# Optimization experiments

Measured on AMD Instinct MI355X. Metric: run time of the kernel, lower is better.

The kernel has to match this reference:

```python
import jax, jax.numpy as jnp
import numpy as np

B, T, NS, NC, M = 256, 128, 12, 4, 6
MU = 0.1                 # barrier parameter alg.mu
REG_BASE = 1.6           # fp.reg_exp_base
REG = 2.0                # bp.reg
REG_FAC = REG_BASE ** REG - 1.0


def _mt(a):
    return jnp.swapaxes(a, -1, -2)


def setup_inputs():
    key = jax.random.key(0)
    k = jax.random.split(key, 18)
    rn = lambda i, shape: jax.random.normal(k[i], shape, dtype=jnp.float32)
    eye_s = jnp.eye(NS, dtype=jnp.float32)
    eye_c = jnp.eye(NC, dtype=jnp.float32)
    fx = 0.9 * eye_s + 0.02 * rn(0, (B, T, NS, NS))
    fu = 0.1 * rn(1, (B, T, NS, NC))
    fxx = 0.01 * rn(2, (B, T, NS, NS, NS))
    fxu = 0.01 * rn(3, (B, T, NS, NS, NC))
    fuu = 0.01 * rn(4, (B, T, NS, NC, NC))
    qx = 0.1 * rn(5, (B, T, NS))
    qu = 0.1 * rn(6, (B, T, NC))
    Ax = 0.1 * rn(7, (B, T, NS, NS))
    qxx = eye_s + Ax @ _mt(Ax)            # PSD stage cost Hessian
    Au = 0.1 * rn(8, (B, T, NC, NC))
    quu = eye_c + Au @ _mt(Au)            # PD control Hessian
    qxu = 0.05 * rn(9, (B, T, NS, NC))
    cx = 0.1 * rn(10, (B, T, M, NS))
    cu = 0.1 * rn(11, (B, T, M, NC))
    # feasible iterate: c < 0 strictly, dual s > 0
    c = -(jax.random.uniform(k[12], (B, T, M), dtype=jnp.float32) + 0.1)
    s = 0.05 + 0.1 * jax.random.uniform(k[13], (B, T, M), dtype=jnp.float32)
    px = 0.1 * rn(14, (B, NS))
    P = 0.1 * rn(15, (B, NS, NS))
    pxx = eye_s + P @ _mt(P)              # PSD terminal Hessian
    return {"qx": qx, "qu": qu, "qxx": qxx, "qxu": qxu, "quu": quu,
            "fx": fx, "fu": fu, "fxx": fxx, "fxu": fxu, "fuu": fuu,
            "cx": cx, "cu": cu, "c": c, "s": s, "px": px, "pxx": pxx}


def _backward_pass(qx, qu, qxx, qxu, quu, fx, fu, fxx, fxu, fuu, cx, cu, c, s, px, pxx):
    """Feasible-branch ipddp Riccati backward recursion over T steps, batched over B."""
    Bsz = qx.shape[0]

    def step(carry, inp):
        Vx, Vxx, dV0, dV1, qu_err, mu_err = carry
        (qx_t, qu_t, qxx_t, qxu_t, quu_t, fx_t, fu_t,
         fxx_t, fxu_t, fuu_t, cx_t, cu_t, c_t, s_t) = inp
        s_col = s_t[..., None]                      # (B,M,1)
        c_col = c_t[..., None]                      # (B,M,1)
        # Q-function expansions
        Qx = qx_t[..., None] + _mt(cx_t) @ s_col + _mt(fx_t) @ Vx       # (B,NS,1)
        Qu = qu_t[..., None] + _mt(cu_t) @ s_col + _mt(fu_t) @ Vx       # (B,NC,1)
        fxV = _mt(fx_t) @ Vxx
        v = Vx[..., 0]                              # (B,NS)
        Qxx = qxx_t + fxV @ fx_t + jnp.einsum('bs,bsij->bij', v, fxx_t)
        Qxu = qxu_t + fxV @ fu_t + jnp.einsum('bs,bsij->bij', v, fxu_t)
        Quu = quu_t + _mt(fu_t) @ Vxx @ fu_t + jnp.einsum('bs,bsij->bij', v, fuu_t)
        Quu = 0.5 * (Quu + _mt(Quu))
        Quu_reg = Quu + quu_t * REG_FAC
        # interior-point (feasible) modifications
        r = s_col * c_col + MU                      # (B,M,1)
        cinv = 1.0 / c_col
        sc = (s_t / c_t)[..., None]                 # diag(SCinv) entries
        SCcu = sc * cu_t                            # SCinv @ cu
        SCcx = sc * cx_t                            # SCinv @ cx
        cuSCcu = _mt(cu_t) @ SCcu
        Qu = Qu - _mt(cu_t) @ (cinv * r)
        tempQux = _mt(Qxu) - _mt(cu_t) @ SCcx       # (B,NC,NS)
        rhs = jnp.concatenate([Qu, tempQux], axis=-1)   # (B,NC,1+NS)
        kK = -jnp.linalg.solve(Quu_reg - cuSCcu, rhs)
        ku = kK[..., :1]                            # (B,NC,1)
        Ku = kK[..., 1:]                            # (B,NC,NS)
        cuku = cu_t @ ku                            # (B,M,1)
        ks = (-cinv * (r + s_col * cuku))[..., 0]   # (B,M)
        Ks = -(sc * (cx_t + cu_t @ Ku))             # (B,M,NS)
        Quu2 = Quu - cuSCcu
        Qxu2 = _mt(tempQux)
        Qxx2 = Qxx - _mt(cx_t) @ SCcx
        Qx2 = Qx - _mt(cx_t) @ (cinv * r)
        dV0 = dV0 + (_mt(ku) @ Qu)[..., 0, 0]
        dV1 = dV1 + 0.5 * (_mt(ku) @ Quu2 @ ku)[..., 0, 0]
        QxuKu = Qxu2 @ Ku
        KtQ = _mt(Ku) @ Quu2
        Vx_new = Qx2 + _mt(Ku) @ Qu + KtQ @ ku + Qxu2 @ ku
        Vxx_new = Qxx2 + _mt(QxuKu) + QxuKu + KtQ @ Ku
        Vxx_new = 0.5 * (Vxx_new + _mt(Vxx_new))
        qu_err = jnp.maximum(qu_err, jnp.max(jnp.abs(Qu)))
        mu_err = jnp.maximum(mu_err, jnp.max(jnp.abs(r)))
        return (Vx_new, Vxx_new, dV0, dV1, qu_err, mu_err), (ku[..., 0], Ku, ks, Ks)

    xs = tuple(jnp.moveaxis(a, 1, 0) for a in
               (qx, qu, qxx, qxu, quu, fx, fu, fxx, fxu, fuu, cx, cu, c, s))
    zero = jnp.zeros((), jnp.float32)
    init = (px[..., None], pxx, jnp.zeros((Bsz,), jnp.float32),
            jnp.zeros((Bsz,), jnp.float32), zero, zero)
    carry, outs = jax.lax.scan(step, init, xs, reverse=True)
    Vx, Vxx, dV0, dV1, qu_err, mu_err = carry
    ku, Ku, ks, Ks = (jnp.moveaxis(o, 0, 1) for o in outs)
    dV = jnp.stack([dV0, dV1], axis=-1)             # (B,2)
    opterr = jnp.maximum(qu_err, mu_err)            # c_err == 0 in feasible branch
    return ku, Ku, ks, Ks, dV, opterr, Vx[..., 0], Vxx


def reference(qx, qu, qxx, qxu, quu, fx, fu, fxx, fxu, fuu, cx, cu, c, s, px, pxx):
    return _backward_pass(qx, qu, qxx, qxu, quu, fx, fu, fxx, fxu, fuu,
                          cx, cu, c, s, px, pxx)
```

## Files before the change

kernel.cpp:

```cpp
#include <hip/hip_runtime.h>
#include <cstdint>
#include <cstddef>

#define B_  256
#define T_  128
#define NS_ 12
#define NC_ 4
#define M_  6

constexpr float MU_F      = 0.1f;
constexpr float REG_FAC_F = (float)(1.6 * 1.6 - 1.0);

#define OF_FX   0
#define OF_FU   144
#define OF_FXX  192
#define OF_FXU  1920
#define OF_FUU  2496
#define OF_QXX  2688
#define OF_QXU  2832
#define OF_QUU  2880
#define OF_QX   2896
#define OF_QU   2908
#define OF_CX   2912
#define OF_CU   2984
#define OF_C    3008
#define OF_S    3014
#define STG_N   3020

#define O_KU    0
#define O_KUBIG 131072
#define O_KS    1703936
#define O_KSBIG 1900544
#define O_DV    4259840
#define O_OPT   4260352
#define O_VX    4260353
#define O_VXX   4263425

__device__ __forceinline__ void bar_lds() {
    asm volatile("s_waitcnt lgkmcnt(0)\n\ts_barrier" ::: "memory");
}

__device__ __forceinline__ void gl_lds16(const float* g, float* l) {
    __builtin_amdgcn_global_load_lds((const __attribute__((address_space(1))) void*)g,
                                     (__attribute__((address_space(3))) void*)l, 16, 0, 0);
}
__device__ __forceinline__ void gl_lds4(const float* g, float* l) {
    __builtin_amdgcn_global_load_lds((const __attribute__((address_space(1))) void*)g,
                                     (__attribute__((address_space(3))) void*)l, 4, 0, 0);
}

__global__ __launch_bounds__(256) void ddp_backward(
    const float* __restrict__ qx,  const float* __restrict__ qu,
    const float* __restrict__ qxx, const float* __restrict__ qxu,
    const float* __restrict__ quu, const float* __restrict__ fx,
    const float* __restrict__ fu,  const float* __restrict__ fxx,
    const float* __restrict__ fxu, const float* __restrict__ fuu,
    const float* __restrict__ cx,  const float* __restrict__ cu,
    const float* __restrict__ c_,  const float* __restrict__ s_,
    const float* __restrict__ px,  const float* __restrict__ pxx,
    float* __restrict__ out, float* __restrict__ ws)
{
    const int tid  = threadIdx.x;
    const int b    = blockIdx.x;
    const int lane = tid & 63;
    const int wv   = tid >> 6;

    __shared__ float stg[2][STG_N];
    __shared__ float sVx[12], sVxx[144];
    __shared__ float sfxV[144], sfuV[48];
    __shared__ float sQxx[144], sQxu[48];
    __shared__ float sQuuR[16], sQuu2[16], sM4[16];
    __shared__ float stQux[48];
    __shared__ float sQxb[12], sQub[4], sQu[4], sQx2[12];
    __shared__ float sr[6], scinv[6], ssc[6];
    __shared__ float sKu[48], sku[4], sKtQ[48];
    __shared__ float sAcc[4];

    const float* srcs[14] = {qx, qu, qxx, qxu, quu, fx, fu, fxx, fxu, fuu, cx, cu, c_, s_};

    auto prefetch = [&](float* dst, int tt) {
        const size_t bt = (size_t)b * T_ + tt;
        constexpr int ch_arr[22]  = {5,6,7,7,7,7,7,7,7,8,8,8,9,2,3,4,0,1,10,11,12,13};
        constexpr int ch_goff[22] = {0,0,0,256,512,768,1024,1280,1536,0,256,512,0,0,0,0,0,0,0,0,0,0};
        constexpr int ch_loff[22] = {OF_FX, OF_FU,
                                     OF_FXX, OF_FXX+256, OF_FXX+512, OF_FXX+768,
                                     OF_FXX+1024, OF_FXX+1280, OF_FXX+1536,
                                     OF_FXU, OF_FXU+256, OF_FXU+512,
                                     OF_FUU, OF_QXX, OF_QXU, OF_QUU, OF_QX, OF_QU,
                                     OF_CX, OF_CU, OF_C, OF_S};
        constexpr int ch_nb[22]   = {576,192,1024,1024,1024,1024,1024,1024,768,
                                     1024,1024,256,768,576,192,64,48,16,288,96,24,24};
        constexpr int sl[14]      = {12,4,144,48,16,144,48,1728,576,192,72,24,6,6};
        #pragma unroll
        for (int ci = 0; ci < 22; ++ci) {
            if ((ci & 3) == wv) {
                const float* g = srcs[ch_arr[ci]] + bt * (size_t)sl[ch_arr[ci]] + ch_goff[ci];
                float* l = dst + ch_loff[ci];
                if ((ch_nb[ci] & 15) == 0) {
                    if (lane * 16 < ch_nb[ci]) gl_lds16(g + lane * 4, l);
                } else {
                    if (lane * 4  < ch_nb[ci]) gl_lds4 (g + lane,     l);
                }
            }
        }
    };

    if (tid < 144) sVxx[tid] = pxx[(size_t)b * 144 + tid];
    if (tid < 12)  sVx[tid]  = px[(size_t)b * 12 + tid];
    if (tid == 0)  { sAcc[0] = 0.f; sAcc[1] = 0.f; sAcc[2] = 0.f; sAcc[3] = 0.f; }
    prefetch(stg[0], T_ - 1);
    __syncthreads();

    int cur = 0;
    for (int t = T_ - 1; t >= 0; --t) {
        const float* S = stg[cur];
        if (t > 0) prefetch(stg[cur ^ 1], t - 1);
        const size_t bt = (size_t)b * T_ + t;

        if (tid < 144) {
            const int i = tid / 12, k = tid % 12;
            float acc = 0.f;
            #pragma unroll
            for (int m = 0; m < 12; ++m) acc += S[OF_FX + m*12 + i] * sVxx[m*12 + k];
            sfxV[tid] = acc;
        } else if (tid < 192) {
            const int idx = tid - 144, a = idx / 12, k = idx % 12;
            float acc = 0.f;
            #pragma unroll
            for (int m = 0; m < 12; ++m) acc += S[OF_FU + m*4 + a] * sVxx[m*12 + k];
            sfuV[idx] = acc;
        } else if (tid < 198) {
            const int k = tid - 192;
            const float cc = S[OF_C + k], ssv = S[OF_S + k];
            sr[k] = ssv * cc + MU_F;
            scinv[k] = 1.0f / cc;
            ssc[k] = ssv / cc;
        } else if (tid < 210) {
            const int i = tid - 198;
            float acc = S[OF_QX + i];
            #pragma unroll
            for (int k = 0; k < 6; ++k)  acc += S[OF_CX + k*12 + i] * S[OF_S + k];
            #pragma unroll
            for (int m = 0; m < 12; ++m) acc += S[OF_FX + m*12 + i] * sVx[m];
            sQxb[i] = acc;
        } else if (tid < 214) {
            const int a = tid - 210;
            float acc = S[OF_QU + a];
            #pragma unroll
            for (int k = 0; k < 6; ++k)  acc += S[OF_CU + k*4 + a] * S[OF_S + k];
            #pragma unroll
            for (int m = 0; m < 12; ++m) acc += S[OF_FU + m*4 + a] * sVx[m];
            sQub[a] = acc;
        }
        bar_lds();

        if (tid < 144) {
            const int i = tid / 12, j = tid % 12; (void)j;
            float acc = S[OF_QXX + tid];
            #pragma unroll
            for (int k = 0; k < 12; ++k) acc += sfxV[i*12 + k] * S[OF_FX + k*12 + (tid % 12)];
            #pragma unroll
            for (int ss2 = 0; ss2 < 12; ++ss2) acc += sVx[ss2] * S[OF_FXX + ss2*144 + tid];
            sQxx[tid] = acc;
        } else if (tid < 192) {
            const int idx = tid - 144, i = idx / 4, j = idx % 4;
            float acc = S[OF_QXU + idx];
            #pragma unroll
            for (int k = 0; k < 12; ++k) acc += sfxV[i*12 + k] * S[OF_FU + k*4 + j];
            #pragma unroll
            for (int ss2 = 0; ss2 < 12; ++ss2) acc += sVx[ss2] * S[OF_FXU + ss2*48 + idx];
            sQxu[idx] = acc;
        } else if (tid < 208) {
            const int idx = tid - 192, a = idx / 4, b2 = idx % 4;
            float acc = S[OF_QUU + idx];
            #pragma unroll
            for (int k = 0; k < 12; ++k) acc += sfuV[a*12 + k] * S[OF_FU + k*4 + b2];
            #pragma unroll
            for (int ss2 = 0; ss2 < 12; ++ss2) acc += sVx[ss2] * S[OF_FUU + ss2*16 + idx];
            sQuuR[idx] = acc;
        }
        bar_lds();

        if (tid < 144) {
            const int i = tid / 12, j = tid % 12;
            float acc = sQxx[tid];
            #pragma unroll
            for (int k = 0; k < 6; ++k) acc -= S[OF_CX + k*12 + i] * ssc[k] * S[OF_CX + k*12 + j];
            sQxx[tid] = acc;
        } else if (tid < 192) {
            const int idx = tid - 144, a = idx / 12, i = idx % 12;
            float acc = sQxu[i*4 + a];
            #pragma unroll
            for (int k = 0; k < 6; ++k) acc -= S[OF_CU + k*4 + a] * ssc[k] * S[OF_CX + k*12 + i];
            stQux[idx] = acc;
        } else if (tid < 208) {
            const int idx = tid - 192, a = idx / 4, b2 = idx % 4;
            const float q = 0.5f * (sQuuR[idx] + sQuuR[b2*4 + a]);
            float cs = 0.f;
            #pragma unroll
            for (int k = 0; k < 6; ++k) cs += ssc[k] * S[OF_CU + k*4 + a] * S[OF_CU + k*4 + b2];
            const float q2 = q - cs;
            sQuu2[idx] = q2;
            sM4[idx]   = q2 + S[OF_QUU + idx] * REG_FAC_F;
        } else if (tid < 212) {
            const int a = tid - 208;
            float acc = sQub[a];
            #pragma unroll
            for (int k = 0; k < 6; ++k) acc -= S[OF_CU + k*4 + a] * scinv[k] * sr[k];
            sQu[a] = acc;
        } else if (tid < 224) {
            const int i = tid - 212;
            float acc = sQxb[i];
            #pragma unroll
            for (int k = 0; k < 6; ++k) acc -= S[OF_CX + k*12 + i] * scinv[k] * sr[k];
            sQx2[i] = acc;
        }
        bar_lds();

        if (tid < 13) {
            float a00=sM4[0],  a01=sM4[1],  a02=sM4[2],  a03=sM4[3];
            float a10=sM4[4],  a11=sM4[5],  a12=sM4[6],  a13=sM4[7];
            float a20=sM4[8],  a21=sM4[9],  a22=sM4[10], a23=sM4[11];
            float a30=sM4[12], a31=sM4[13], a32=sM4[14], a33=sM4[15];
            const float i0 = 1.0f / a00;
            const float l10 = a10*i0, l20 = a20*i0, l30 = a30*i0;
            a11 -= l10*a01; a12 -= l10*a02; a13 -= l10*a03;
            a21 -= l20*a01; a22 -= l20*a02; a23 -= l20*a03;
            a31 -= l30*a01; a32 -= l30*a02; a33 -= l30*a03;
            const float i1 = 1.0f / a11;
            const float l21 = a21*i1, l31 = a31*i1;
            a22 -= l21*a12; a23 -= l21*a13;
            a32 -= l31*a12; a33 -= l31*a13;
            const float i2 = 1.0f / a22;
            const float l32 = a32*i2;
            a33 -= l32*a23;

            float r0, r1, r2, r3;
            if (tid == 0) { r0 = sQu[0]; r1 = sQu[1]; r2 = sQu[2]; r3 = sQu[3]; }
            else { const int i = tid - 1; r0 = stQux[i]; r1 = stQux[12+i]; r2 = stQux[24+i]; r3 = stQux[36+i]; }

            const float y0 = r0;
            const float y1 = r1 - l10*y0;
            const float y2 = r2 - l20*y0 - l21*y1;
            const float y3 = r3 - l30*y0 - l31*y1 - l32*y2;
            float x3 = y3 / a33;
            float x2 = (y2 - a23*x3) * i2;
            float x1 = (y1 - a12*x2 - a13*x3) * i1;
            float x0 = (y0 - a01*x1 - a02*x2 - a03*x3) * i0;
            x0 = -x0; x1 = -x1; x2 = -x2; x3 = -x3;

            if (tid == 0) {
                sku[0]=x0; sku[1]=x1; sku[2]=x2; sku[3]=x3;
                float* kg = out + O_KU + bt*4;
                kg[0]=x0; kg[1]=x1; kg[2]=x2; kg[3]=x3;
            } else {
                const int i = tid - 1;
                sKu[i]=x0; sKu[12+i]=x1; sKu[24+i]=x2; sKu[36+i]=x3;
                float* Kg = out + O_KUBIG + bt*48;
                Kg[i]=x0; Kg[12+i]=x1; Kg[24+i]=x2; Kg[36+i]=x3;
            }
        }
        bar_lds();

        if (tid < 48) {
            const int i = tid / 4, a = tid % 4;
            float acc = 0.f;
            #pragma unroll
            for (int b2 = 0; b2 < 4; ++b2) acc += sKu[b2*12 + i] * sQuu2[b2*4 + a];
            sKtQ[tid] = acc;
        } else if (tid < 54) {
            const int k = tid - 48;
            float cuku = 0.f;
            #pragma unroll
            for (int a = 0; a < 4; ++a) cuku += S[OF_CU + k*4 + a] * sku[a];
            out[O_KS + bt*6 + k] = -scinv[k] * (sr[k] + S[OF_S + k] * cuku);
        } else if (tid < 126) {
            const int idx = tid - 54, k = idx / 12, i = idx % 12;
            float acc = S[OF_CX + k*12 + i];
            #pragma unroll
            for (int a = 0; a < 4; ++a) acc += S[OF_CU + k*4 + a] * sKu[a*12 + i];
            out[O_KSBIG + bt*72 + idx] = -(ssc[k] * acc);
        } else if (tid == 126) {
            float d = 0.f;
            #pragma unroll
            for (int a = 0; a < 4; ++a) d += sku[a] * sQu[a];
            sAcc[0] += d;
        } else if (tid == 127) {
            float d = 0.f;
            #pragma unroll
            for (int a = 0; a < 4; ++a)
                #pragma unroll
                for (int b2 = 0; b2 < 4; ++b2) d += sku[a] * sQuu2[a*4 + b2] * sku[b2];
            sAcc[1] += 0.5f * d;
        } else if (tid == 128) {
            float m = 0.f;
            #pragma unroll
            for (int a = 0; a < 4; ++a) m = fmaxf(m, fabsf(sQu[a]));
            sAcc[2] = fmaxf(sAcc[2], m);
        } else if (tid == 129) {
            float m = 0.f;
            #pragma unroll
            for (int k = 0; k < 6; ++k) m = fmaxf(m, fabsf(sr[k]));
            sAcc[3] = fmaxf(sAcc[3], m);
        }
        bar_lds();

        if (tid < 144) {
            const int i = tid / 12, j = tid % 12;
            const float v1 = sQxx[i*12 + j], v2 = sQxx[j*12 + i];
            float qk = 0.f, kk1 = 0.f, kk2 = 0.f;
            #pragma unroll
            for (int a = 0; a < 4; ++a) {
                const float kui = sKu[a*12 + i], kuj = sKu[a*12 + j];
                qk  += stQux[a*12 + i] * kuj + stQux[a*12 + j] * kui;
                kk1 += sKtQ[i*4 + a] * kuj;
                kk2 += sKtQ[j*4 + a] * kui;
            }
            sVxx[tid] = 0.5f * (v1 + v2) + qk + 0.5f * (kk1 + kk2);
        } else if (tid < 156) {
            const int i = tid - 144;
            float acc = sQx2[i];
            #pragma unroll
            for (int a = 0; a < 4; ++a)
                acc += sKu[a*12 + i] * sQu[a] + sKtQ[i*4 + a] * sku[a] + stQux[a*12 + i] * sku[a];
            sVx[i] = acc;
        }
        __syncthreads();
        cur ^= 1;
    }

    if (tid == 0) {
        out[O_DV + b*2 + 0] = sAcc[0];
        out[O_DV + b*2 + 1] = sAcc[1];
        ws[b] = fmaxf(sAcc[2], sAcc[3]);
    }
    if (tid < 12)  out[O_VX + b*12 + tid] = sVx[tid];
    if (tid < 144) out[O_VXX + (size_t)b*144 + tid] = sVxx[tid];
}

__global__ __launch_bounds__(256) void opt_reduce(const float* __restrict__ ws,
                                                  float* __restrict__ out)
{
    float v = ws[threadIdx.x];
    #pragma unroll
    for (int o = 32; o > 0; o >>= 1) v = fmaxf(v, __shfl_down(v, o, 64));
    __shared__ float m[4];
    if ((threadIdx.x & 63) == 0) m[threadIdx.x >> 6] = v;
    __syncthreads();
    if (threadIdx.x == 0) out[O_OPT] = fmaxf(fmaxf(m[0], m[1]), fmaxf(m[2], m[3]));
}

extern "C" void kernel_launch(void* const* d_in, const int* in_sizes, int n_in,
                              void* d_out, int out_size, void* d_ws, size_t ws_size,
                              hipStream_t stream) {
    const float* qx  = (const float*)d_in[0];
    const float* qu  = (const float*)d_in[1];
    const float* qxx = (const float*)d_in[2];
    const float* qxu = (const float*)d_in[3];
    const float* quu = (const float*)d_in[4];
    const float* fx  = (const float*)d_in[5];
    const float* fu  = (const float*)d_in[6];
    const float* fxx = (const float*)d_in[7];
    const float* fxu = (const float*)d_in[8];
    const float* fuu = (const float*)d_in[9];
    const float* cx  = (const float*)d_in[10];
    const float* cu  = (const float*)d_in[11];
    const float* c_  = (const float*)d_in[12];
    const float* s_  = (const float*)d_in[13];
    const float* px  = (const float*)d_in[14];
    const float* pxx = (const float*)d_in[15];
    float* out = (float*)d_out;
    float* ws  = (float*)d_ws;

    hipLaunchKernelGGL(ddp_backward, dim3(B_), dim3(256), 0, stream,
                       qx, qu, qxx, qxu, quu, fx, fu, fxx, fxu, fuu,
                       cx, cu, c_, s_, px, pxx, out, ws);
    hipLaunchKernelGGL(opt_reduce, dim3(1), dim3(256), 0, stream, ws, out);
}
```

Measured before the change: 805.2 us.

## Collapse per-batch Riccati block to a single wavefront with fused phases

```diff
diff --git a/kernel.cpp b/kernel.cpp
--- a/kernel.cpp
+++ b/kernel.cpp
@@ -4,9 +4,6 @@
 
 #define B_  256
 #define T_  128
-#define NS_ 12
-#define NC_ 4
-#define M_  6
 
 constexpr float MU_F      = 0.1f;
 constexpr float REG_FAC_F = (float)(1.6 * 1.6 - 1.0);
@@ -36,10 +33,6 @@
 #define O_VX    4260353
 #define O_VXX   4263425
 
-__device__ __forceinline__ void bar_lds() {
-    asm volatile("s_waitcnt lgkmcnt(0)\n\ts_barrier" ::: "memory");
-}
-
 __device__ __forceinline__ void gl_lds16(const float* g, float* l) {
     __builtin_amdgcn_global_load_lds((const __attribute__((address_space(1))) void*)g,
                                      (__attribute__((address_space(3))) void*)l, 16, 0, 0);
@@ -48,8 +41,11 @@
     __builtin_amdgcn_global_load_lds((const __attribute__((address_space(1))) void*)g,
                                      (__attribute__((address_space(3))) void*)l, 4, 0, 0);
 }
-
-__global__ __launch_bounds__(256) void ddp_backward(
+__device__ __forceinline__ void wait_vm0() {
+    asm volatile("s_waitcnt vmcnt(0)" ::: "memory");
+}
+
+__global__ __launch_bounds__(64) void ddp_backward(
     const float* __restrict__ qx,  const float* __restrict__ qu,
     const float* __restrict__ qxx, const float* __restrict__ qxu,
     const float* __restrict__ quu, const float* __restrict__ fx,
@@ -60,25 +56,23 @@
     const float* __restrict__ px,  const float* __restrict__ pxx,
     float* __restrict__ out, float* __restrict__ ws)
 {
-    const int tid  = threadIdx.x;
+    const int lane = threadIdx.x;
     const int b    = blockIdx.x;
-    const int lane = tid & 63;
-    const int wv   = tid >> 6;
 
     __shared__ float stg[2][STG_N];
     __shared__ float sVx[12], sVxx[144];
     __shared__ float sfxV[144], sfuV[48];
-    __shared__ float sQxx[144], sQxu[48];
-    __shared__ float sQuuR[16], sQuu2[16], sM4[16];
-    __shared__ float stQux[48];
+    __shared__ float sQxx2[144], stQux[48], sGuu[16];
     __shared__ float sQxb[12], sQub[4], sQu[4], sQx2[12];
-    __shared__ float sr[6], scinv[6], ssc[6];
-    __shared__ float sKu[48], sku[4], sKtQ[48];
-    __shared__ float sAcc[4];
+    __shared__ float sr[6], scinv[6], ssc[6], sscr[6];
+    __shared__ float sKu[48], sku[4];
+    __shared__ float sErr[2];
+
+    float accDV0 = 0.f, accDV1 = 0.f, accQE = 0.f, accME = 0.f;
 
     const float* srcs[14] = {qx, qu, qxx, qxu, quu, fx, fu, fxx, fxu, fuu, cx, cu, c_, s_};
 
-    auto prefetch = [&](float* dst, int tt) {
+    auto stage_all = [&](float* dst, int tt) {
         const size_t bt = (size_t)b * T_ + tt;
         constexpr int ch_arr[22]  = {5,6,7,7,7,7,7,7,7,8,8,8,9,2,3,4,0,1,10,11,12,13};
         constexpr int ch_goff[22] = {0,0,0,256,512,768,1024,1280,1536,0,256,512,0,0,0,0,0,0,0,0,0,0};
@@ -93,249 +87,252 @@
         constexpr int sl[14]      = {12,4,144,48,16,144,48,1728,576,192,72,24,6,6};
         #pragma unroll
         for (int ci = 0; ci < 22; ++ci) {
-            if ((ci & 3) == wv) {
-                const float* g = srcs[ch_arr[ci]] + bt * (size_t)sl[ch_arr[ci]] + ch_goff[ci];
-                float* l = dst + ch_loff[ci];
-                if ((ch_nb[ci] & 15) == 0) {
-                    if (lane * 16 < ch_nb[ci]) gl_lds16(g + lane * 4, l);
-                } else {
-                    if (lane * 4  < ch_nb[ci]) gl_lds4 (g + lane,     l);
-                }
+            const float* g = srcs[ch_arr[ci]] + bt * (size_t)sl[ch_arr[ci]] + ch_goff[ci];
+            float* l = dst + ch_loff[ci];
+            if ((ch_nb[ci] & 15) == 0) {
+                if (lane * 16 < ch_nb[ci]) gl_lds16(g + lane * 4, l);
+            } else {
+                if (lane * 4  < ch_nb[ci]) gl_lds4 (g + lane,     l);
             }
         }
     };
 
-    if (tid < 144) sVxx[tid] = pxx[(size_t)b * 144 + tid];
-    if (tid < 12)  sVx[tid]  = px[(size_t)b * 12 + tid];
-    if (tid == 0)  { sAcc[0] = 0.f; sAcc[1] = 0.f; sAcc[2] = 0.f; sAcc[3] = 0.f; }
-    prefetch(stg[0], T_ - 1);
+    for (int e = lane; e < 144; e += 64) sVxx[e] = pxx[(size_t)b * 144 + e];
+    if (lane < 12) sVx[lane] = px[(size_t)b * 12 + lane];
+    stage_all(stg[0], T_ - 1);
+    wait_vm0();
     __syncthreads();
 
     int cur = 0;
     for (int t = T_ - 1; t >= 0; --t) {
         const float* S = stg[cur];
-        if (t > 0) prefetch(stg[cur ^ 1], t - 1);
+        if (t > 0) stage_all(stg[cur ^ 1], t - 1);
         const size_t bt = (size_t)b * T_ + t;
 
-        if (tid < 144) {
-            const int i = tid / 12, k = tid % 12;
-            float acc = 0.f;
-            #pragma unroll
-            for (int m = 0; m < 12; ++m) acc += S[OF_FX + m*12 + i] * sVxx[m*12 + k];
-            sfxV[tid] = acc;
-        } else if (tid < 192) {
-            const int idx = tid - 144, a = idx / 12, k = idx % 12;
-            float acc = 0.f;
-            #pragma unroll
-            for (int m = 0; m < 12; ++m) acc += S[OF_FU + m*4 + a] * sVxx[m*12 + k];
-            sfuV[idx] = acc;
-        } else if (tid < 198) {
-            const int k = tid - 192;
-            const float cc = S[OF_C + k], ssv = S[OF_S + k];
-            sr[k] = ssv * cc + MU_F;
-            scinv[k] = 1.0f / cc;
-            ssc[k] = ssv / cc;
-        } else if (tid < 210) {
-            const int i = tid - 198;
-            float acc = S[OF_QX + i];
-            #pragma unroll
-            for (int k = 0; k < 6; ++k)  acc += S[OF_CX + k*12 + i] * S[OF_S + k];
-            #pragma unroll
-            for (int m = 0; m < 12; ++m) acc += S[OF_FX + m*12 + i] * sVx[m];
-            sQxb[i] = acc;
-        } else if (tid < 214) {
-            const int a = tid - 210;
-            float acc = S[OF_QU + a];
-            #pragma unroll
-            for (int k = 0; k < 6; ++k)  acc += S[OF_CU + k*4 + a] * S[OF_S + k];
-            #pragma unroll
-            for (int m = 0; m < 12; ++m) acc += S[OF_FU + m*4 + a] * sVx[m];
-            sQub[a] = acc;
-        }
-        bar_lds();
-
-        if (tid < 144) {
-            const int i = tid / 12, j = tid % 12; (void)j;
-            float acc = S[OF_QXX + tid];
-            #pragma unroll
-            for (int k = 0; k < 12; ++k) acc += sfxV[i*12 + k] * S[OF_FX + k*12 + (tid % 12)];
-            #pragma unroll
-            for (int ss2 = 0; ss2 < 12; ++ss2) acc += sVx[ss2] * S[OF_FXX + ss2*144 + tid];
-            sQxx[tid] = acc;
-        } else if (tid < 192) {
-            const int idx = tid - 144, i = idx / 4, j = idx % 4;
-            float acc = S[OF_QXU + idx];
-            #pragma unroll
-            for (int k = 0; k < 12; ++k) acc += sfxV[i*12 + k] * S[OF_FU + k*4 + j];
-            #pragma unroll
-            for (int ss2 = 0; ss2 < 12; ++ss2) acc += sVx[ss2] * S[OF_FXU + ss2*48 + idx];
-            sQxu[idx] = acc;
-        } else if (tid < 208) {
-            const int idx = tid - 192, a = idx / 4, b2 = idx % 4;
-            float acc = S[OF_QUU + idx];
-            #pragma unroll
-            for (int k = 0; k < 12; ++k) acc += sfuV[a*12 + k] * S[OF_FU + k*4 + b2];
-            #pragma unroll
-            for (int ss2 = 0; ss2 < 12; ++ss2) acc += sVx[ss2] * S[OF_FUU + ss2*16 + idx];
-            sQuuR[idx] = acc;
-        }
-        bar_lds();
-
-        if (tid < 144) {
-            const int i = tid / 12, j = tid % 12;
-            float acc = sQxx[tid];
-            #pragma unroll
-            for (int k = 0; k < 6; ++k) acc -= S[OF_CX + k*12 + i] * ssc[k] * S[OF_CX + k*12 + j];
-            sQxx[tid] = acc;
-        } else if (tid < 192) {
-            const int idx = tid - 144, a = idx / 12, i = idx % 12;
-            float acc = sQxu[i*4 + a];
-            #pragma unroll
-            for (int k = 0; k < 6; ++k) acc -= S[OF_CU + k*4 + a] * ssc[k] * S[OF_CX + k*12 + i];
-            stQux[idx] = acc;
-        } else if (tid < 208) {
-            const int idx = tid - 192, a = idx / 4, b2 = idx % 4;
-            const float q = 0.5f * (sQuuR[idx] + sQuuR[b2*4 + a]);
-            float cs = 0.f;
-            #pragma unroll
-            for (int k = 0; k < 6; ++k) cs += ssc[k] * S[OF_CU + k*4 + a] * S[OF_CU + k*4 + b2];
-            const float q2 = q - cs;
-            sQuu2[idx] = q2;
-            sM4[idx]   = q2 + S[OF_QUU + idx] * REG_FAC_F;
-        } else if (tid < 212) {
-            const int a = tid - 208;
-            float acc = sQub[a];
-            #pragma unroll
-            for (int k = 0; k < 6; ++k) acc -= S[OF_CU + k*4 + a] * scinv[k] * sr[k];
-            sQu[a] = acc;
-        } else if (tid < 224) {
-            const int i = tid - 212;
-            float acc = sQxb[i];
-            #pragma unroll
-            for (int k = 0; k < 6; ++k) acc -= S[OF_CX + k*12 + i] * scinv[k] * sr[k];
-            sQx2[i] = acc;
-        }
-        bar_lds();
-
-        if (tid < 13) {
-            float a00=sM4[0],  a01=sM4[1],  a02=sM4[2],  a03=sM4[3];
-            float a10=sM4[4],  a11=sM4[5],  a12=sM4[6],  a13=sM4[7];
-            float a20=sM4[8],  a21=sM4[9],  a22=sM4[10], a23=sM4[11];
-            float a30=sM4[12], a31=sM4[13], a32=sM4[14], a33=sM4[15];
-            const float i0 = 1.0f / a00;
-            const float l10 = a10*i0, l20 = a20*i0, l30 = a30*i0;
-            a11 -= l10*a01; a12 -= l10*a02; a13 -= l10*a03;
-            a21 -= l20*a01; a22 -= l20*a02; a23 -= l20*a03;
-            a31 -= l30*a01; a32 -= l30*a02; a33 -= l30*a03;
-            const float i1 = 1.0f / a11;
-            const float l21 = a21*i1, l31 = a31*i1;
-            a22 -= l21*a12; a23 -= l21*a13;
-            a32 -= l31*a12; a33 -= l31*a13;
-            const float i2 = 1.0f / a22;
-            const float l32 = a32*i2;
-            a33 -= l32*a23;
-
-            float r0, r1, r2, r3;
-            if (tid == 0) { r0 = sQu[0]; r1 = sQu[1]; r2 = sQu[2]; r3 = sQu[3]; }
-            else { const int i = tid - 1; r0 = stQux[i]; r1 = stQux[12+i]; r2 = stQux[24+i]; r3 = stQux[36+i]; }
-
-            const float y0 = r0;
-            const float y1 = r1 - l10*y0;
-            const float y2 = r2 - l20*y0 - l21*y1;
-            const float y3 = r3 - l30*y0 - l31*y1 - l32*y2;
-            float x3 = y3 / a33;
-            float x2 = (y2 - a23*x3) * i2;
-            float x1 = (y1 - a12*x2 - a13*x3) * i1;
-            float x0 = (y0 - a01*x1 - a02*x2 - a03*x3) * i0;
-            x0 = -x0; x1 = -x1; x2 = -x2; x3 = -x3;
-
-            if (tid == 0) {
-                sku[0]=x0; sku[1]=x1; sku[2]=x2; sku[3]=x3;
-                float* kg = out + O_KU + bt*4;
-                kg[0]=x0; kg[1]=x1; kg[2]=x2; kg[3]=x3;
+        {
+            const float* wp; int wss; float* op; int k0;
+            if (lane < 48) {
+                const int i = lane >> 2; k0 = (lane & 3) * 3;
+                wp = S + OF_FX + i; wss = 12; op = sfxV + i * 12 + k0;
             } else {
-                const int i = tid - 1;
-                sKu[i]=x0; sKu[12+i]=x1; sKu[24+i]=x2; sKu[36+i]=x3;
-                float* Kg = out + O_KUBIG + bt*48;
-                Kg[i]=x0; Kg[12+i]=x1; Kg[24+i]=x2; Kg[36+i]=x3;
-            }
-        }
-        bar_lds();
-
-        if (tid < 48) {
-            const int i = tid / 4, a = tid % 4;
-            float acc = 0.f;
-            #pragma unroll
-            for (int b2 = 0; b2 < 4; ++b2) acc += sKu[b2*12 + i] * sQuu2[b2*4 + a];
-            sKtQ[tid] = acc;
-        } else if (tid < 54) {
-            const int k = tid - 48;
-            float cuku = 0.f;
-            #pragma unroll
-            for (int a = 0; a < 4; ++a) cuku += S[OF_CU + k*4 + a] * sku[a];
-            out[O_KS + bt*6 + k] = -scinv[k] * (sr[k] + S[OF_S + k] * cuku);
-        } else if (tid < 126) {
-            const int idx = tid - 54, k = idx / 12, i = idx % 12;
-            float acc = S[OF_CX + k*12 + i];
-            #pragma unroll
-            for (int a = 0; a < 4; ++a) acc += S[OF_CU + k*4 + a] * sKu[a*12 + i];
-            out[O_KSBIG + bt*72 + idx] = -(ssc[k] * acc);
-        } else if (tid == 126) {
+                const int a = (lane - 48) >> 2; k0 = ((lane - 48) & 3) * 3;
+                wp = S + OF_FU + a; wss = 4;  op = sfuV + a * 12 + k0;
+            }
+            float a0 = 0.f, a1 = 0.f, a2 = 0.f;
+            #pragma unroll
+            for (int m = 0; m < 12; ++m) {
+                const float w = wp[m * wss];
+                const float* vp = sVxx + m * 12 + k0;
+                a0 += w * vp[0]; a1 += w * vp[1]; a2 += w * vp[2];
+            }
+            op[0] = a0; op[1] = a1; op[2] = a2;
+        }
+        if (lane < 6) {
+            const int k = lane;
+            const float cc = S[OF_C + k], sv = S[OF_S + k];
+            const float r  = sv * cc + MU_F;
+            const float ci = 1.0f / cc;
+            sr[k] = r; scinv[k] = ci; ssc[k] = sv * ci; sscr[k] = ci * r;
+        } else if (lane < 22) {
+            const float* cp; int cs; const float* fp; int fs; float bias; float* o;
+            if (lane < 18) { const int i = lane - 6;  cp = S + OF_CX + i; cs = 12; fp = S + OF_FX + i; fs = 12; bias = S[OF_QX + i]; o = sQxb + i; }
+            else           { const int a = lane - 18; cp = S + OF_CU + a; cs = 4;  fp = S + OF_FU + a; fs = 4;  bias = S[OF_QU + a]; o = sQub + a; }
+            float acc = bias;
+            #pragma unroll
+            for (int k = 0; k < 6; ++k)  acc += cp[k * cs] * S[OF_S + k];
+            #pragma unroll
+            for (int m = 0; m < 12; ++m) acc += fp[m * fs] * sVx[m];
+            *o = acc;
+        }
+        __syncthreads();
+
+        {
+            const float *wp; int wss; const float *op; int osk, osd;
+            const float *pp; int pss, psd; const float *up; int uss;
+            const float *vp; const float *bp; int bsd; float *outp;
+            if (lane < 48) {
+                const int i = lane >> 2, j0 = (lane & 3) * 3;
+                wp = sfxV + i * 12;           wss = 1;
+                op = S + OF_FX + j0;          osk = 12; osd = 1;
+                pp = S + OF_FXX + i * 12 + j0; pss = 144; psd = 1;
+                up = S + OF_CX + i;           uss = 12;
+                vp = S + OF_CX + j0;
+                bp = S + OF_QXX + i * 12 + j0; bsd = 1;
+                outp = sQxx2 + i * 12 + j0;
+            } else {
+                const int a = (lane - 48) >> 2, i0 = ((lane - 48) & 3) * 3;
+                wp = S + OF_FU + a;           wss = 4;
+                op = sfxV + i0 * 12;          osk = 1;  osd = 12;
+                pp = S + OF_FXU + i0 * 4 + a; pss = 48; psd = 4;
+                up = S + OF_CU + a;           uss = 4;
+                vp = S + OF_CX + i0;
+                bp = S + OF_QXU + i0 * 4 + a; bsd = 4;
+                outp = stQux + a * 12 + i0;
+            }
+            float e0 = bp[0], e1 = bp[bsd], e2 = bp[2 * bsd];
+            #pragma unroll
+            for (int k = 0; k < 12; ++k) {
+                const float w = wp[k * wss];
+                const float* o = op + k * osk;
+                e0 += w * o[0]; e1 += w * o[osd]; e2 += w * o[2 * osd];
+            }
+            #pragma unroll
+            for (int s2 = 0; s2 < 12; ++s2) {
+                const float v = sVx[s2];
+                const float* p = pp + s2 * pss;
+                e0 += v * p[0]; e1 += v * p[psd]; e2 += v * p[2 * psd];
+            }
+            #pragma unroll
+            for (int k = 0; k < 6; ++k) {
+                const float tt = ssc[k] * up[k * uss];
+                const float* v = vp + k * 12;
+                e0 -= tt * v[0]; e1 -= tt * v[1]; e2 -= tt * v[2];
+            }
+            outp[0] = e0; outp[1] = e1; outp[2] = e2;
+        }
+        if (lane < 16) {
+            const int a = lane >> 2, b2 = lane & 3;
+            float acc = S[OF_QUU + lane];
+            #pragma unroll
+            for (int k = 0; k < 12; ++k)  acc += sfuV[a * 12 + k] * S[OF_FU + k * 4 + b2];
+            #pragma unroll
+            for (int s2 = 0; s2 < 12; ++s2) acc += sVx[s2] * S[OF_FUU + s2 * 16 + lane];
+            #pragma unroll
+            for (int k = 0; k < 6; ++k)   acc -= ssc[k] * S[OF_CU + k * 4 + a] * S[OF_CU + k * 4 + b2];
+            sGuu[lane] = acc;
+        } else if (lane < 32) {
+            const float* cp; int cs; float bias; float* o;
+            if (lane < 20) { const int a = lane - 16; cp = S + OF_CU + a; cs = 4;  bias = sQub[a]; o = sQu + a; }
+            else           { const int i = lane - 20; cp = S + OF_CX + i; cs = 12; bias = sQxb[i]; o = sQx2 + i; }
+            float acc = bias;
+            #pragma unroll
+            for (int k = 0; k < 6; ++k) acc -= cp[k * cs] * sscr[k];
+            *o = acc;
+        }
+        __syncthreads();
+
+        float q2v[16];
+        {
+            float m4[16];
+            #pragma unroll
+            for (int e = 0; e < 16; ++e) {
+                const int a = e >> 2, b2 = e & 3;
+                const float g = 0.5f * (sGuu[e] + sGuu[b2 * 4 + a]);
+                q2v[e] = g;
+                m4[e]  = g + S[OF_QUU + e] * REG_FAC_F;
+            }
+            const float i0  = 1.0f / m4[0];
+            const float l10 = m4[4] * i0, l20 = m4[8] * i0, l30 = m4[12] * i0;
+            float a11 = m4[5]  - l10 * m4[1], a12 = m4[6]  - l10 * m4[2], a13 = m4[7]  - l10 * m4[3];
+            float a21 = m4[9]  - l20 * m4[1], a22 = m4[10] - l20 * m4[2], a23 = m4[11] - l20 * m4[3];
+            float a31 = m4[13] - l30 * m4[1], a32 = m4[14] - l30 * m4[2], a33 = m4[15] - l30 * m4[3];
+            const float i1  = 1.0f / a11;
+            const float l21 = a21 * i1, l31 = a31 * i1;
+            a22 -= l21 * a12; a23 -= l21 * a13;
+            a32 -= l31 * a12; a33 -= l31 * a13;
+            const float i2  = 1.0f / a22;
+            const float l32 = a32 * i2;
+            a33 -= l32 * a23;
+
+            if (lane < 13) {
+                const int ii = (lane == 0) ? 0 : (lane - 1);
+                float r0, r1, r2, r3;
+                if (lane == 0) { r0 = sQu[0]; r1 = sQu[1]; r2 = sQu[2]; r3 = sQu[3]; }
+                else { r0 = stQux[ii]; r1 = stQux[12 + ii]; r2 = stQux[24 + ii]; r3 = stQux[36 + ii]; }
+                const float y0 = r0;
+                const float y1 = r1 - l10 * y0;
+                const float y2 = r2 - l20 * y0 - l21 * y1;
+                const float y3 = r3 - l30 * y0 - l31 * y1 - l32 * y2;
+                float x3 = y3 / a33;
+                float x2 = (y2 - a23 * x3) * i2;
+                float x1 = (y1 - a12 * x2 - a13 * x3) * i1;
+                float x0 = (y0 - m4[1] * x1 - m4[2] * x2 - m4[3] * x3) * i0;
+                x0 = -x0; x1 = -x1; x2 = -x2; x3 = -x3;
+
+                const int gst = (lane == 0) ? 1 : 12;
+                float* lK = (lane == 0) ? sku : (sKu + ii);
+                lK[0] = x0; lK[gst] = x1; lK[2 * gst] = x2; lK[3 * gst] = x3;
+                float* gK = (lane == 0) ? (out + O_KU + bt * 4) : (out + O_KUBIG + bt * 48 + ii);
+                gK[0] = x0; gK[gst] = x1; gK[2 * gst] = x2; gK[3 * gst] = x3;
+
+                const float* w1p = (lane == 0) ? scinv : ssc;
+                const float* bpp = (lane == 0) ? sr : (S + OF_CX + ii);
+                const int    bst = (lane == 0) ? 1 : 12;
+                float* gS = (lane == 0) ? (out + O_KS + bt * 6) : (out + O_KSBIG + bt * 72 + ii);
+                #pragma unroll
+                for (int k = 0; k < 6; ++k) {
+                    const float tsum = S[OF_CU + k*4] * x0 + S[OF_CU + k*4 + 1] * x1
+                                     + S[OF_CU + k*4 + 2] * x2 + S[OF_CU + k*4 + 3] * x3;
+                    const float w2 = (lane == 0) ? S[OF_S + k] : 1.0f;
+                    gS[k * gst] = -w1p[k] * (bpp[k * bst] + w2 * tsum);
+                }
+            }
+        }
+        __syncthreads();
+
+        if (lane < 48) {
+            const int i = lane >> 2, j0 = (lane & 3) * 3;
+            float kcol[4], tq[4], kt[4];
+            #pragma unroll
+            for (int a2 = 0; a2 < 4; ++a2) { kcol[a2] = sKu[a2 * 12 + i]; tq[a2] = stQux[a2 * 12 + i]; }
+            #pragma unroll
+            for (int a2 = 0; a2 < 4; ++a2)
+                kt[a2] = kcol[0] * q2v[a2] + kcol[1] * q2v[4 + a2] + kcol[2] * q2v[8 + a2] + kcol[3] * q2v[12 + a2];
+            #pragma unroll
+            for (int d = 0; d < 3; ++d) {
+                const int j = j0 + d;
+                float acc = 0.5f * (sQxx2[i * 12 + j] + sQxx2[j * 12 + i]);
+                #pragma unroll
+                for (int a2 = 0; a2 < 4; ++a2) {
+                    const float kj = sKu[a2 * 12 + j];
+                    acc += tq[a2] * kj + stQux[a2 * 12 + j] * kcol[a2] + kt[a2] * kj;
+                }
+                sVxx[i * 12 + j] = acc;
+            }
+        } else if (lane < 60) {
+            const int i = lane - 48;
+            const float kc0 = sKu[i], kc1 = sKu[12 + i], kc2 = sKu[24 + i], kc3 = sKu[36 + i];
+            float acc = sQx2[i] + kc0 * sQu[0] + kc1 * sQu[1] + kc2 * sQu[2] + kc3 * sQu[3];
+            #pragma unroll
+            for (int a2 = 0; a2 < 4; ++a2) {
+                const float kta = kc0 * q2v[a2] + kc1 * q2v[4 + a2] + kc2 * q2v[8 + a2] + kc3 * q2v[12 + a2];
+                acc += (kta + stQux[a2 * 12 + i]) * sku[a2];
+            }
+            sVx[i] = acc;
+        } else if (lane == 60) {
+            accDV0 += sku[0] * sQu[0] + sku[1] * sQu[1] + sku[2] * sQu[2] + sku[3] * sQu[3];
+        } else if (lane == 61) {
             float d = 0.f;
             #pragma unroll
-            for (int a = 0; a < 4; ++a) d += sku[a] * sQu[a];
-            sAcc[0] += d;
-        } else if (tid == 127) {
-            float d = 0.f;
-            #pragma unroll
-            for (int a = 0; a < 4; ++a)
-                #pragma unroll
-                for (int b2 = 0; b2 < 4; ++b2) d += sku[a] * sQuu2[a*4 + b2] * sku[b2];
-            sAcc[1] += 0.5f * d;
-        } else if (tid == 128) {
+            for (int a2 = 0; a2 < 4; ++a2) {
+                float tb = q2v[a2 * 4] * sku[0] + q2v[a2 * 4 + 1] * sku[1]
+                         + q2v[a2 * 4 + 2] * sku[2] + q2v[a2 * 4 + 3] * sku[3];
+                d += sku[a2] * tb;
+            }
+            accDV1 += 0.5f * d;
+        } else if (lane == 62) {
+            float m = fabsf(sQu[0]);
+            m = fmaxf(m, fabsf(sQu[1])); m = fmaxf(m, fabsf(sQu[2])); m = fmaxf(m, fabsf(sQu[3]));
+            accQE = fmaxf(accQE, m);
+        } else {
             float m = 0.f;
             #pragma unroll
-            for (int a = 0; a < 4; ++a) m = fmaxf(m, fabsf(sQu[a]));
-            sAcc[2] = fmaxf(sAcc[2], m);
-        } else if (tid == 129) {
-            float m = 0.f;
-            #pragma unroll
             for (int k = 0; k < 6; ++k) m = fmaxf(m, fabsf(sr[k]));
-            sAcc[3] = fmaxf(sAcc[3], m);
-        }
-        bar_lds();
-
-        if (tid < 144) {
-            const int i = tid / 12, j = tid % 12;
-            const float v1 = sQxx[i*12 + j], v2 = sQxx[j*12 + i];
-            float qk = 0.f, kk1 = 0.f, kk2 = 0.f;
-            #pragma unroll
-            for (int a = 0; a < 4; ++a) {
-                const float kui = sKu[a*12 + i], kuj = sKu[a*12 + j];
-                qk  += stQux[a*12 + i] * kuj + stQux[a*12 + j] * kui;
-                kk1 += sKtQ[i*4 + a] * kuj;
-                kk2 += sKtQ[j*4 + a] * kui;
-            }
-            sVxx[tid] = 0.5f * (v1 + v2) + qk + 0.5f * (kk1 + kk2);
-        } else if (tid < 156) {
-            const int i = tid - 144;
-            float acc = sQx2[i];
-            #pragma unroll
-            for (int a = 0; a < 4; ++a)
-                acc += sKu[a*12 + i] * sQu[a] + sKtQ[i*4 + a] * sku[a] + stQux[a*12 + i] * sku[a];
-            sVx[i] = acc;
-        }
+            accME = fmaxf(accME, m);
+        }
+        wait_vm0();
         __syncthreads();
         cur ^= 1;
     }
 
-    if (tid == 0) {
-        out[O_DV + b*2 + 0] = sAcc[0];
-        out[O_DV + b*2 + 1] = sAcc[1];
-        ws[b] = fmaxf(sAcc[2], sAcc[3]);
-    }
-    if (tid < 12)  out[O_VX + b*12 + tid] = sVx[tid];
-    if (tid < 144) out[O_VXX + (size_t)b*144 + tid] = sVxx[tid];
+    if (lane == 60) out[O_DV + b * 2 + 0] = accDV0;
+    if (lane == 61) out[O_DV + b * 2 + 1] = accDV1;
+    if (lane == 62) sErr[0] = accQE;
+    if (lane == 63) sErr[1] = accME;
+    __syncthreads();
+    if (lane == 0) ws[b] = fmaxf(sErr[0], sErr[1]);
+    if (lane < 12) out[O_VX + b * 12 + lane] = sVx[lane];
+    for (int e = lane; e < 144; e += 64) out[O_VXX + (size_t)b * 144 + e] = sVxx[e];
 }
 
 __global__ __launch_bounds__(256) void opt_reduce(const float* __restrict__ ws,
@@ -372,7 +369,7 @@
     float* out = (float*)d_out;
     float* ws  = (float*)d_ws;
 
-    hipLaunchKernelGGL(ddp_backward, dim3(B_), dim3(256), 0, stream,
+    hipLaunchKernelGGL(ddp_backward, dim3(B_), dim3(64), 0, stream,
                        qx, qu, qxx, qxu, quu, fx, fu, fxx, fxu, fuu,
                        cx, cu, c_, s_, px, pxx, out, ws);
     hipLaunchKernelGGL(opt_reduce, dim3(1), dim3(256), 0, stream, ws, out);
```

New measurement: 860.6 us. 1.07x slower.
